# Kernel optimization log

Measured on AMD Instinct MI355X. Metric: run time of the kernel, lower is better.

Reference implementation:

```python
import jax, jax.numpy as jnp
import numpy as np

NUM_HEADS = 8
CHUNK = 64
TOP_K = 5


def setup_inputs() -> dict:
    key = jax.random.key(0)
    ks = jax.random.split(key, 5)
    D = 512
    x = jax.random.normal(ks[0], (1, 2048, D), dtype=jnp.float32)
    s = 0.02
    Wq = jax.random.normal(ks[1], (D, D), dtype=jnp.float32) * s
    Wk = jax.random.normal(ks[2], (D, D), dtype=jnp.float32) * s
    Wv = jax.random.normal(ks[3], (D, D), dtype=jnp.float32) * s
    Wo = jax.random.normal(ks[4], (D, D), dtype=jnp.float32) * s
    return {"x": x, "Wq": Wq, "Wk": Wk, "Wv": Wv, "Wo": Wo}


def reference(x, Wq, Wk, Wv, Wo):
    B, S, D = x.shape
    H = NUM_HEADS
    hd = D // H
    scale = hd ** -0.5
    C = S // CHUNK  # number of chunks

    def split_heads(t):
        return t.reshape(B, S, H, hd).transpose(0, 2, 1, 3)  # [B,H,S,hd]

    Q = split_heads(x @ Wq)
    K = split_heads(x @ Wk)
    V = split_heads(x @ Wv)

    # chunked K/V: [B,H,C,chunk,hd]
    Kc = K.reshape(B, H, C, CHUNK, hd)
    Vc = V.reshape(B, H, C, CHUNK, hd)

    # chunk descriptors: mean-pooled keys per chunk -> [B,H,C,hd]
    chunk_keys = Kc.mean(axis=3)

    # route each query to top-k chunks by scaled similarity
    sims = jnp.einsum('bhsd,bhcd->bhsc', Q, chunk_keys) * scale  # [B,H,S,C]
    _, idx = jax.lax.top_k(sims, TOP_K)  # [B,H,S,K]

    # gather selected K/V chunk blocks: [B,H,S,K,chunk,hd]
    idx_flat = idx.reshape(B, H, S * TOP_K)[:, :, :, None, None]
    Kg = jnp.take_along_axis(Kc, idx_flat, axis=2).reshape(B, H, S, TOP_K, CHUNK, hd)
    Vg = jnp.take_along_axis(Vc, idx_flat, axis=2).reshape(B, H, S, TOP_K, CHUNK, hd)

    # sparse block attention over the K*chunk gathered keys per query
    scores = jnp.einsum('bhsd,bhskcd->bhskc', Q, Kg) * scale
    attn = jax.nn.softmax(scores.reshape(B, H, S, TOP_K * CHUNK), axis=-1)
    attn = attn.reshape(B, H, S, TOP_K, CHUNK)
    out = jnp.einsum('bhskc,bhskcd->bhsd', attn, Vg)  # [B,H,S,hd]

    out = out.transpose(0, 2, 1, 3).reshape(B, S, D)
    return out @ Wo
```

## Files before the change

### kernel.cpp

```cpp
#include <hip/hip_runtime.h>
#include <hip/hip_bf16.h>
#include <math.h>

#define S_LEN 2048
#define D_DIM 512
#define H_NUM 8
#define HD    64
#define C_NUM 32
#define TOPK  5
#define SCALE 0.125f
#define QCAP  1024
#define ATILES 16

typedef __attribute__((ext_vector_type(8))) short bf16x8;
typedef __attribute__((ext_vector_type(4))) float f32x4;
typedef __attribute__((ext_vector_type(4))) unsigned short us4;

__device__ __forceinline__ unsigned short f2b(float f) {
    __hip_bfloat16 h = __float2bfloat16(f);
    unsigned short u;
    __builtin_memcpy(&u, &h, 2);
    return u;
}
__device__ __forceinline__ bf16x8 pack8(float4 a, float4 b) {
    bf16x8 r;
    r[0] = (short)f2b(a.x); r[1] = (short)f2b(a.y);
    r[2] = (short)f2b(a.z); r[3] = (short)f2b(a.w);
    r[4] = (short)f2b(b.x); r[5] = (short)f2b(b.y);
    r[6] = (short)f2b(b.z); r[7] = (short)f2b(b.w);
    return r;
}
__device__ __forceinline__ float b2f(unsigned short u) {
    __hip_bfloat16 h;
    __builtin_memcpy(&h, &u, 2);
    return __bfloat162float(h);
}

#define BM 64
#define BN 64
#define BK 32

__device__ __forceinline__ void gemm_body(const float* __restrict__ A,
                                          const float* __restrict__ B,
                                          float* __restrict__ C,
                                          int M, int N, int K,
                                          int bx, int by) {
    __shared__ float As[BK][BM + 4];
    __shared__ float Bs[BK][BN];

    const int t  = threadIdx.x;
    const int tx = t & 15;
    const int ty = t >> 4;
    const int m0 = by * BM;
    const int n0 = bx * BN;

    float4 acc0 = make_float4(0.f,0.f,0.f,0.f);
    float4 acc1 = make_float4(0.f,0.f,0.f,0.f);
    float4 acc2 = make_float4(0.f,0.f,0.f,0.f);
    float4 acc3 = make_float4(0.f,0.f,0.f,0.f);

    const int ar = t >> 3;
    const int ac = (t & 7) * 4;
    const int br = t >> 4;
    const int bc = (t & 15) * 4;

    float4 a0, a1, b0, b1;
    auto LD = [&](int k0) {
        a0 = *(const float4*)&A[(size_t)(m0 + ar)      * K + k0 + ac];
        a1 = *(const float4*)&A[(size_t)(m0 + ar + 32) * K + k0 + ac];
        b0 = *(const float4*)&B[(size_t)(k0 + br)      * N + n0 + bc];
        b1 = *(const float4*)&B[(size_t)(k0 + br + 16) * N + n0 + bc];
    };

    LD(0);
    for (int k0 = 0; k0 < K; k0 += BK) {
        __syncthreads();
        As[ac+0][ar]    = a0.x; As[ac+1][ar]    = a0.y; As[ac+2][ar]    = a0.z; As[ac+3][ar]    = a0.w;
        As[ac+0][ar+32] = a1.x; As[ac+1][ar+32] = a1.y; As[ac+2][ar+32] = a1.z; As[ac+3][ar+32] = a1.w;
        *(float4*)&Bs[br][bc]      = b0;
        *(float4*)&Bs[br + 16][bc] = b1;
        __syncthreads();

        if (k0 + BK < K) LD(k0 + BK);

        #pragma unroll
        for (int kk = 0; kk < BK; ++kk) {
            float4 a = *(const float4*)&As[kk][ty * 4];
            float4 b = *(const float4*)&Bs[kk][tx * 4];
            acc0.x += a.x*b.x; acc0.y += a.x*b.y; acc0.z += a.x*b.z; acc0.w += a.x*b.w;
            acc1.x += a.y*b.x; acc1.y += a.y*b.y; acc1.z += a.y*b.z; acc1.w += a.y*b.w;
            acc2.x += a.z*b.x; acc2.y += a.z*b.y; acc2.z += a.z*b.z; acc2.w += a.z*b.w;
            acc3.x += a.w*b.x; acc3.y += a.w*b.y; acc3.z += a.w*b.z; acc3.w += a.w*b.w;
        }
    }

    *(float4*)&C[(size_t)(m0 + ty*4 + 0) * N + n0 + tx*4] = acc0;
    *(float4*)&C[(size_t)(m0 + ty*4 + 1) * N + n0 + tx*4] = acc1;
    *(float4*)&C[(size_t)(m0 + ty*4 + 2) * N + n0 + tx*4] = acc2;
    *(float4*)&C[(size_t)(m0 + ty*4 + 3) * N + n0 + tx*4] = acc3;
}

__global__ __launch_bounds__(256) void gemm_qkv(const float* __restrict__ A,
                                                const float* __restrict__ Wq,
                                                const float* __restrict__ Wk,
                                                float* __restrict__ Qb,
                                                float* __restrict__ Kb) {
    const float* B = (blockIdx.z == 0) ? Wq : Wk;
    float*       C = (blockIdx.z == 0) ? Qb : Kb;
    gemm_body(A, B, C, S_LEN, D_DIM, D_DIM, blockIdx.x, blockIdx.y);
}

template <bool ABF16, bool CBF16>
__device__ __forceinline__ void gemm_bf16_body(const void* __restrict__ Aptr,
                                               const float* __restrict__ B,
                                               void* __restrict__ Cptr,
                                               int M, int N, int K,
                                               int bx, int by) {
    __shared__ unsigned short As[64][72];
    __shared__ unsigned short Bs[64][72];

    const int t  = threadIdx.x;
    const int m0 = by * 64;
    const int n0 = bx * 64;
    const int rl = t >> 2;
    const int c4 = (t & 3) * 16;

    const int lane = t & 63, w = t >> 6, lr = lane & 15, quad = lane >> 4;

    f32x4 acc[4] = {{0.f,0.f,0.f,0.f},{0.f,0.f,0.f,0.f},
                    {0.f,0.f,0.f,0.f},{0.f,0.f,0.f,0.f}};

    float4 fa[4]; bf16x8 ba[2]; float4 fb[4];
    auto LDA = [&](int k0) {
        if (ABF16) {
            const unsigned short* A = (const unsigned short*)Aptr;
            ba[0] = *(const bf16x8*)&A[(size_t)(m0 + rl) * K + k0 + c4];
            ba[1] = *(const bf16x8*)&A[(size_t)(m0 + rl) * K + k0 + c4 + 8];
        } else {
            const float* A = (const float*)Aptr;
            const float* p = &A[(size_t)(m0 + rl) * K + k0 + c4];
            fa[0] = *(const float4*)&p[0];  fa[1] = *(const float4*)&p[4];
            fa[2] = *(const float4*)&p[8];  fa[3] = *(const float4*)&p[12];
        }
    };
    auto LDB = [&](int k0) {
        const float* p = &B[(size_t)(k0 + rl) * N + n0 + c4];
        fb[0] = *(const float4*)&p[0];  fb[1] = *(const float4*)&p[4];
        fb[2] = *(const float4*)&p[8];  fb[3] = *(const float4*)&p[12];
    };

    LDA(0); LDB(0);
    for (int k0 = 0; k0 < K; k0 += 64) {
        __syncthreads();
        if (ABF16) {
            *(bf16x8*)&As[rl][c4]     = ba[0];
            *(bf16x8*)&As[rl][c4 + 8] = ba[1];
        } else {
            *(bf16x8*)&As[rl][c4]     = pack8(fa[0], fa[1]);
            *(bf16x8*)&As[rl][c4 + 8] = pack8(fa[2], fa[3]);
        }
        #pragma unroll
        for (int f = 0; f < 4; ++f) {
            float4 v = fb[f];
            Bs[c4 + f*4 + 0][rl] = f2b(v.x);
            Bs[c4 + f*4 + 1][rl] = f2b(v.y);
            Bs[c4 + f*4 + 2][rl] = f2b(v.z);
            Bs[c4 + f*4 + 3][rl] = f2b(v.w);
        }
        __syncthreads();

        if (k0 + 64 < K) { LDA(k0 + 64); LDB(k0 + 64); }

        bf16x8 a0 = *(const bf16x8*)&As[w * 16 + lr][quad * 8];
        bf16x8 a1 = *(const bf16x8*)&As[w * 16 + lr][32 + quad * 8];
        #pragma unroll
        for (int nt = 0; nt < 4; ++nt) {
            bf16x8 b0 = *(const bf16x8*)&Bs[nt * 16 + lr][quad * 8];
            bf16x8 b1 = *(const bf16x8*)&Bs[nt * 16 + lr][32 + quad * 8];
            acc[nt] = __builtin_amdgcn_mfma_f32_16x16x32_bf16(a0, b0, acc[nt], 0, 0, 0);
            acc[nt] = __builtin_amdgcn_mfma_f32_16x16x32_bf16(a1, b1, acc[nt], 0, 0, 0);
        }
    }

    #pragma unroll
    for (int nt = 0; nt < 4; ++nt)
        #pragma unroll
        for (int r = 0; r < 4; ++r) {
            int m = m0 + w * 16 + quad * 4 + r;
            int n = n0 + nt * 16 + lr;
            if (CBF16) ((unsigned short*)Cptr)[(size_t)m * N + n] = f2b(acc[nt][r]);
            else       ((float*)Cptr)[(size_t)m * N + n] = acc[nt][r];
        }
}

__global__ __launch_bounds__(256) void gemm_v(const float* __restrict__ x,
                                              const float* __restrict__ Wv,
                                              unsigned short* __restrict__ Vbf,
                                              int* __restrict__ cur) {
    if (blockIdx.x == 0 && blockIdx.y == 0) cur[threadIdx.x] = 0;
    gemm_bf16_body<false, true>(x, Wv, Vbf, S_LEN, D_DIM, D_DIM,
                                blockIdx.x, blockIdx.y);
}

__global__ __launch_bounds__(256) void gemm_out(const unsigned short* __restrict__ Obn,
                                                const float* __restrict__ Wo,
                                                float* __restrict__ out) {
    gemm_bf16_body<true, false>(Obn, Wo, out, S_LEN, D_DIM, D_DIM,
                                blockIdx.x, blockIdx.y);
}

__global__ __launch_bounds__(256) void chunk_keys_kernel(const float* __restrict__ K,
                                                         float* __restrict__ ck) {
    int i = blockIdx.x * 256 + threadIdx.x;
    int c = i >> 9;
    int d = i & 511;
    const float* p = K + (size_t)c * 64 * D_DIM + d;
    float sum = 0.f;
    #pragma unroll
    for (int r = 0; r < 64; ++r) sum += p[(size_t)r * D_DIM];
    ck[(size_t)c * D_DIM + d] = sum * (1.0f / 64.0f);
}

__global__ __launch_bounds__(256) void sims_topk(const float* __restrict__ Q,
                                                 const float* __restrict__ ck,
                                                 int* __restrict__ cur,
                                                 unsigned short* __restrict__ qlist) {
    __shared__ float qtile[64][68];
    __shared__ float cks[32][68];
    __shared__ float simsb[64][36];
    __shared__ int   lds_cnt[32];
    __shared__ int   lds_base[32];

    const int t  = threadIdx.x;
    const int s0 = blockIdx.x * 64;
    const int h  = blockIdx.y;

    if (t < 32) lds_cnt[t] = 0;

    {
        int r = t >> 2;
        #pragma unroll
        for (int i = 0; i < 4; ++i) {
            int cf4 = (t & 3) * 4 + i;
            *(float4*)&qtile[r][cf4 * 4] =
                *(const float4*)&Q[(size_t)(s0 + r) * D_DIM + h * HD + cf4 * 4];
        }
    }
    for (int i = t; i < C_NUM * 16; i += 256) {
        int c = i >> 4, df4 = i & 15;
        *(float4*)&cks[c][df4 * 4] =
            *(const float4*)&ck[(size_t)c * D_DIM + h * HD + df4 * 4];
    }
    __syncthreads();

    {
        const int sl = t >> 2, g = t & 3;
        float sa[8] = {0.f,0.f,0.f,0.f,0.f,0.f,0.f,0.f};
        #pragma unroll
        for (int d4 = 0; d4 < 16; ++d4) {
            float4 q4 = *(const float4*)&qtile[sl][d4 * 4];
            #pragma unroll
            for (int j = 0; j < 8; ++j) {
                float4 c4 = *(const float4*)&cks[g * 8 + j][d4 * 4];
                sa[j] += q4.x*c4.x + q4.y*c4.y + q4.z*c4.z + q4.w*c4.w;
            }
        }
        *(float4*)&simsb[sl][g*8 + 0] = make_float4(sa[0], sa[1], sa[2], sa[3]);
        *(float4*)&simsb[sl][g*8 + 4] = make_float4(sa[4], sa[5], sa[6], sa[7]);
    }
    __syncthreads();

    int csel[TOPK], lpos[TOPK];
    if (t < 64) {
        float sv[32];
        #pragma unroll
        for (int cq = 0; cq < 8; ++cq) {
            float4 v = *(const float4*)&simsb[t][cq * 4];
            sv[cq*4+0] = v.x; sv[cq*4+1] = v.y; sv[cq*4+2] = v.z; sv[cq*4+3] = v.w;
        }
        #pragma unroll
        for (int k = 0; k < TOPK; ++k) {
            float best = -INFINITY; int bi = 0;
            #pragma unroll
            for (int cc = 0; cc < 32; ++cc) {
                bool gt = sv[cc] > best;
                best = gt ? sv[cc] : best;
                bi   = gt ? cc : bi;
            }
            #pragma unroll
            for (int cc = 0; cc < 32; ++cc)
                if (cc == bi) sv[cc] = -INFINITY;
            csel[k] = bi;
            lpos[k] = atomicAdd(&lds_cnt[bi], 1);
        }
    }
    __syncthreads();

    if (t < 32) lds_base[t] = atomicAdd(&cur[h * 32 + t], lds_cnt[t]);
    __syncthreads();

    if (t < 64) {
        #pragma unroll
        for (int k = 0; k < TOPK; ++k) {
            int c = csel[k];
            int pos = lds_base[c] + lpos[k];
            if (pos < QCAP)
                qlist[(size_t)(h * 32 + c) * QCAP + pos] =
                    (unsigned short)((s0 + t) | (k << 11));
        }
    }
}

__global__ __launch_bounds__(256) void moc_attn6(const float* __restrict__ Q,
                                                 const float* __restrict__ K,
                                                 const unsigned short* __restrict__ Vbf,
                                                 const int* __restrict__ cnt,
                                                 const unsigned short* __restrict__ qlist,
                                                 float* __restrict__ lpart,
                                                 float* __restrict__ Opart) {
    __shared__ unsigned short Qs[64][72];
    __shared__ unsigned short Ks[64][72];
    __shared__ unsigned short VT[64][72];
    __shared__ unsigned short Ps[64][72];
    __shared__ unsigned short slist[64];

    const int hc = blockIdx.y;
    const int h  = hc >> 5;
    const int c  = hc & 31;
    const int g  = blockIdx.x;
    const int t  = threadIdx.x;

    const int count = min(cnt[hc], QCAP);
    const int base  = g * 64;
    if (base >= count) return;
    const int lim = min(count - base, 64);

    const float* Kb = K + ((size_t)c * 64) * D_DIM + h * HD;
    const unsigned short* Vb = Vbf + ((size_t)c * 64) * D_DIM + h * HD;
    const unsigned short* list = qlist + (size_t)hc * QCAP + base;

    {
        const int j  = t >> 2;
        const int d0 = (t & 3) * 16;

        const float* kr = Kb + (size_t)j * D_DIM + d0;
        float4 k0 = *(const float4*)&kr[0],  k1 = *(const float4*)&kr[4];
        float4 k2 = *(const float4*)&kr[8],  k3 = *(const float4*)&kr[12];
        *(bf16x8*)&Ks[j][d0]     = pack8(k0, k1);
        *(bf16x8*)&Ks[j][d0 + 8] = pack8(k2, k3);

        const unsigned short* vr = Vb + (size_t)j * D_DIM + d0;
        bf16x8 v0 = *(const bf16x8*)&vr[0];
        bf16x8 v1 = *(const bf16x8*)&vr[8];
        #pragma unroll
        for (int i = 0; i < 8; ++i) {
            VT[d0 + i][j]     = (unsigned short)v0[i];
            VT[d0 + 8 + i][j] = (unsigned short)v1[i];
        }

        unsigned short pv = (j < lim) ? list[j] : (unsigned short)0xFFFF;
        if ((t & 3) == 0) slist[j] = pv;
        int s = (pv == 0xFFFF) ? 0 : (int)(pv & 2047);
        const float* qr = Q + (size_t)s * D_DIM + h * HD + d0;
        float4 q0 = *(const float4*)&qr[0],  q1 = *(const float4*)&qr[4];
        float4 q2 = *(const float4*)&qr[8],  q3 = *(const float4*)&qr[12];
        *(bf16x8*)&Qs[j][d0]     = pack8(q0, q1);
        *(bf16x8*)&Qs[j][d0 + 8] = pack8(q2, q3);
    }
    __syncthreads();

    const int lane = t & 63;
    const int w    = t >> 6;
    const int lr   = lane & 15;
    const int quad = lane >> 4;

    bf16x8 aq0 = *(const bf16x8*)&Qs[w * 16 + lr][quad * 8];
    bf16x8 aq1 = *(const bf16x8*)&Qs[w * 16 + lr][32 + quad * 8];

    f32x4 acc[4];
    #pragma unroll
    for (int kt = 0; kt < 4; ++kt) {
        bf16x8 b0 = *(const bf16x8*)&Ks[kt * 16 + lr][quad * 8];
        bf16x8 b1 = *(const bf16x8*)&Ks[kt * 16 + lr][32 + quad * 8];
        f32x4 z = {0.f, 0.f, 0.f, 0.f};
        z = __builtin_amdgcn_mfma_f32_16x16x32_bf16(aq0, b0, z, 0, 0, 0);
        z = __builtin_amdgcn_mfma_f32_16x16x32_bf16(aq1, b1, z, 0, 0, 0);
        acc[kt] = z;
    }

    unsigned short pb[4][4];
    float dsum[4] = {0.f, 0.f, 0.f, 0.f};
    #pragma unroll
    for (int kt = 0; kt < 4; ++kt) {
        #pragma unroll
        for (int r = 0; r < 4; ++r) {
            unsigned short u = f2b(__expf(acc[kt][r] * SCALE));
            pb[kt][r] = u;
            dsum[r] += b2f(u);
        }
    }
    #pragma unroll
    for (int r = 0; r < 4; ++r) {
        float v = dsum[r];
        v += __shfl_xor(v, 1, 64);
        v += __shfl_xor(v, 2, 64);
        v += __shfl_xor(v, 4, 64);
        v += __shfl_xor(v, 8, 64);
        dsum[r] = v;
    }
    if (lr == 0) {
        #pragma unroll
        for (int r = 0; r < 4; ++r) {
            unsigned short sv = slist[w * 16 + quad * 4 + r];
            if (sv != 0xFFFF) {
                int kk = sv >> 11, s = sv & 2047;
                lpart[((size_t)kk * H_NUM + h) * S_LEN + s] = dsum[r];
            }
        }
    }

    #pragma unroll
    for (int kt = 0; kt < 4; ++kt)
        #pragma unroll
        for (int r = 0; r < 4; ++r)
            Ps[w * 16 + quad * 4 + r][kt * 16 + lr] = pb[kt][r];

    bf16x8 ap0 = *(const bf16x8*)&Ps[w * 16 + lr][quad * 8];
    bf16x8 ap1 = *(const bf16x8*)&Ps[w * 16 + lr][32 + quad * 8];

    #pragma unroll
    for (int dt = 0; dt < 4; ++dt) {
        bf16x8 b0 = *(const bf16x8*)&VT[dt * 16 + lr][quad * 8];
        bf16x8 b1 = *(const bf16x8*)&VT[dt * 16 + lr][32 + quad * 8];
        f32x4 z = {0.f, 0.f, 0.f, 0.f};
        z = __builtin_amdgcn_mfma_f32_16x16x32_bf16(ap0, b0, z, 0, 0, 0);
        z = __builtin_amdgcn_mfma_f32_16x16x32_bf16(ap1, b1, z, 0, 0, 0);
        #pragma unroll
        for (int r = 0; r < 4; ++r) {
            unsigned short sv = slist[w * 16 + quad * 4 + r];
            if (sv != 0xFFFF) {
                int kk = sv >> 11, s = sv & 2047;
                Opart[((((size_t)kk * H_NUM + h) * S_LEN + s) * HD) + dt * 16 + lr] = z[r];
            }
        }
    }
}

__global__ __launch_bounds__(256) void reduce_norm(const float4* __restrict__ Opart4,
                                                   const float* __restrict__ lpart,
                                                   unsigned short* __restrict__ Obn) {
    int i = blockIdx.x * 256 + threadIdx.x;
    int s    = i >> 7;
    int col4 = i & 127;
    int h    = col4 >> 4;
    int f4   = col4 & 15;
    float4 acc = make_float4(0.f,0.f,0.f,0.f);
    float  den = 0.f;
    #pragma unroll
    for (int k = 0; k < TOPK; ++k) {
        size_t slot = ((size_t)k * H_NUM + h) * S_LEN + s;
        float4 v = Opart4[slot * 16 + f4];
        acc.x += v.x; acc.y += v.y; acc.z += v.z; acc.w += v.w;
        den += lpart[slot];
    }
    float inv = 1.0f / den;
    us4 o;
    o[0] = f2b(acc.x * inv); o[1] = f2b(acc.y * inv);
    o[2] = f2b(acc.z * inv); o[3] = f2b(acc.w * inv);
    *(us4*)&Obn[(size_t)i * 4] = o;
}

extern "C" void kernel_launch(void* const* d_in, const int* in_sizes, int n_in,
                              void* d_out, int out_size, void* d_ws, size_t ws_size,
                              hipStream_t stream) {
    const float* x  = (const float*)d_in[0];
    const float* Wq = (const float*)d_in[1];
    const float* Wk = (const float*)d_in[2];
    const float* Wv = (const float*)d_in[3];
    const float* Wo = (const float*)d_in[4];
    float* out = (float*)d_out;

    const size_t SD = (size_t)S_LEN * D_DIM;
    float* ws    = (float*)d_ws;
    float* Qb    = ws;
    float* Kb    = Qb + SD;
    unsigned short* Vbf = (unsigned short*)(Kb + SD);
    float* ck    = (float*)(Vbf + SD);
    float* lpart = ck + (size_t)C_NUM * D_DIM;
    int*   curb  = (int*)(lpart + (size_t)TOPK * H_NUM * S_LEN);
    unsigned short* qlst = (unsigned short*)(curb + 256);
    float* Opart = (float*)(qlst + (size_t)256 * QCAP);
    unsigned short* Obn = (unsigned short*)Qb;

    dim3 qkgrid(D_DIM / BN, S_LEN / BM, 2);
    gemm_qkv<<<qkgrid, 256, 0, stream>>>(x, Wq, Wk, Qb, Kb);

    dim3 vgrid(D_DIM / 64, S_LEN / 64);
    gemm_v<<<vgrid, 256, 0, stream>>>(x, Wv, Vbf, curb);

    chunk_keys_kernel<<<(C_NUM * D_DIM) / 256, 256, 0, stream>>>(Kb, ck);

    dim3 rgrid(S_LEN / 64, H_NUM);
    sims_topk<<<rgrid, 256, 0, stream>>>(Qb, ck, curb, qlst);

    dim3 agrid(ATILES, H_NUM * C_NUM);
    moc_attn6<<<agrid, 256, 0, stream>>>(Qb, Kb, Vbf, curb, qlst, lpart, Opart);

    reduce_norm<<<(int)(SD / 4 / 256), 256, 0, stream>>>((const float4*)Opart, lpart, Obn);

    dim3 ogrid(D_DIM / 64, S_LEN / 64);
    gemm_out<<<ogrid, 256, 0, stream>>>(Obn, Wo, out);
}
```

Measured before the change: 159.2 us.

## Double-buffer fp32 GEMM shared tiles and merge V projection into QK launch

The fp32 Q/K GEMM now uses two shared-memory buffers, so the next tile is stored while the current one is used, leaving one barrier per k-step instead of two. The separate V projection kernel is merged into the Q/K launch as a third grid slice (blockIdx.z==2), which removes one kernel launch and lets the three projections run at the same time. The cost is double the shared memory in the fp32 path, which may lower occupancy. The merged kernel also declares the shared arrays of both GEMM bodies, which may raise LDS use per block.

```diff
diff --git a/kernel.cpp b/kernel.cpp
--- a/kernel.cpp
+++ b/kernel.cpp
@@ -45,8 +45,8 @@
                                           float* __restrict__ C,
                                           int M, int N, int K,
                                           int bx, int by) {
-    __shared__ float As[BK][BM + 4];
-    __shared__ float Bs[BK][BN];
+    __shared__ float As[2][BK][BM + 4];
+    __shared__ float Bs[2][BK][BN];
 
     const int t  = threadIdx.x;
     const int tx = t & 15;
@@ -71,43 +71,39 @@
         b0 = *(const float4*)&B[(size_t)(k0 + br)      * N + n0 + bc];
         b1 = *(const float4*)&B[(size_t)(k0 + br + 16) * N + n0 + bc];
     };
-
-    LD(0);
+    auto ST = [&](int p) {
+        As[p][ac+0][ar]    = a0.x; As[p][ac+1][ar]    = a0.y; As[p][ac+2][ar]    = a0.z; As[p][ac+3][ar]    = a0.w;
+        As[p][ac+0][ar+32] = a1.x; As[p][ac+1][ar+32] = a1.y; As[p][ac+2][ar+32] = a1.z; As[p][ac+3][ar+32] = a1.w;
+        *(float4*)&Bs[p][br][bc]      = b0;
+        *(float4*)&Bs[p][br + 16][bc] = b1;
+    };
+
+    LD(0); ST(0); __syncthreads();
+
+    int p = 0;
     for (int k0 = 0; k0 < K; k0 += BK) {
-        __syncthreads();
-        As[ac+0][ar]    = a0.x; As[ac+1][ar]    = a0.y; As[ac+2][ar]    = a0.z; As[ac+3][ar]    = a0.w;
-        As[ac+0][ar+32] = a1.x; As[ac+1][ar+32] = a1.y; As[ac+2][ar+32] = a1.z; As[ac+3][ar+32] = a1.w;
-        *(float4*)&Bs[br][bc]      = b0;
-        *(float4*)&Bs[br + 16][bc] = b1;
-        __syncthreads();
-
-        if (k0 + BK < K) LD(k0 + BK);
+        const bool more = (k0 + BK < K);
+        if (more) LD(k0 + BK);
 
         #pragma unroll
         for (int kk = 0; kk < BK; ++kk) {
-            float4 a = *(const float4*)&As[kk][ty * 4];
-            float4 b = *(const float4*)&Bs[kk][tx * 4];
+            float4 a = *(const float4*)&As[p][kk][ty * 4];
+            float4 b = *(const float4*)&Bs[p][kk][tx * 4];
             acc0.x += a.x*b.x; acc0.y += a.x*b.y; acc0.z += a.x*b.z; acc0.w += a.x*b.w;
             acc1.x += a.y*b.x; acc1.y += a.y*b.y; acc1.z += a.y*b.z; acc1.w += a.y*b.w;
             acc2.x += a.z*b.x; acc2.y += a.z*b.y; acc2.z += a.z*b.z; acc2.w += a.z*b.w;
             acc3.x += a.w*b.x; acc3.y += a.w*b.y; acc3.z += a.w*b.z; acc3.w += a.w*b.w;
         }
+
+        if (more) ST(p ^ 1);
+        __syncthreads();
+        p ^= 1;
     }
 
     *(float4*)&C[(size_t)(m0 + ty*4 + 0) * N + n0 + tx*4] = acc0;
     *(float4*)&C[(size_t)(m0 + ty*4 + 1) * N + n0 + tx*4] = acc1;
     *(float4*)&C[(size_t)(m0 + ty*4 + 2) * N + n0 + tx*4] = acc2;
     *(float4*)&C[(size_t)(m0 + ty*4 + 3) * N + n0 + tx*4] = acc3;
-}
-
-__global__ __launch_bounds__(256) void gemm_qkv(const float* __restrict__ A,
-                                                const float* __restrict__ Wq,
-                                                const float* __restrict__ Wk,
-                                                float* __restrict__ Qb,
-                                                float* __restrict__ Kb) {
-    const float* B = (blockIdx.z == 0) ? Wq : Wk;
-    float*       C = (blockIdx.z == 0) ? Qb : Kb;
-    gemm_body(A, B, C, S_LEN, D_DIM, D_DIM, blockIdx.x, blockIdx.y);
 }
 
 template <bool ABF16, bool CBF16>
@@ -193,13 +189,23 @@
         }
 }
 
-__global__ __launch_bounds__(256) void gemm_v(const float* __restrict__ x,
-                                              const float* __restrict__ Wv,
-                                              unsigned short* __restrict__ Vbf,
-                                              int* __restrict__ cur) {
-    if (blockIdx.x == 0 && blockIdx.y == 0) cur[threadIdx.x] = 0;
-    gemm_bf16_body<false, true>(x, Wv, Vbf, S_LEN, D_DIM, D_DIM,
-                                blockIdx.x, blockIdx.y);
+__global__ __launch_bounds__(256) void gemm_qkv(const float* __restrict__ x,
+                                                const float* __restrict__ Wq,
+                                                const float* __restrict__ Wk,
+                                                const float* __restrict__ Wv,
+                                                float* __restrict__ Qb,
+                                                float* __restrict__ Kb,
+                                                unsigned short* __restrict__ Vbf,
+                                                int* __restrict__ cur) {
+    if (blockIdx.z == 2) {
+        if (blockIdx.x == 0 && blockIdx.y == 0) cur[threadIdx.x] = 0;
+        gemm_bf16_body<false, true>(x, Wv, Vbf, S_LEN, D_DIM, D_DIM,
+                                    blockIdx.x, blockIdx.y);
+        return;
+    }
+    const float* B = (blockIdx.z == 0) ? Wq : Wk;
+    float*       C = (blockIdx.z == 0) ? Qb : Kb;
+    gemm_body(x, B, C, S_LEN, D_DIM, D_DIM, blockIdx.x, blockIdx.y);
 }
 
 __global__ __launch_bounds__(256) void gemm_out(const unsigned short* __restrict__ Obn,
@@ -492,11 +498,8 @@
     float* Opart = (float*)(qlst + (size_t)256 * QCAP);
     unsigned short* Obn = (unsigned short*)Qb;
 
-    dim3 qkgrid(D_DIM / BN, S_LEN / BM, 2);
-    gemm_qkv<<<qkgrid, 256, 0, stream>>>(x, Wq, Wk, Qb, Kb);
-
-    dim3 vgrid(D_DIM / 64, S_LEN / 64);
-    gemm_v<<<vgrid, 256, 0, stream>>>(x, Wv, Vbf, curb);
+    dim3 qkvgrid(D_DIM / BN, S_LEN / BM, 3);
+    gemm_qkv<<<qkvgrid, 256, 0, stream>>>(x, Wq, Wk, Wv, Qb, Kb, Vbf, curb);
 
     chunk_keys_kernel<<<(C_NUM * D_DIM) / 256, 256, 0, stream>>>(Kb, ck);
 
```

After: 169.1 us. 1.06x slower.

## Double-buffer A tile in LDS and stream B directly from global in registers

Applied to the files above, without the earlier changes.

The fp32 GEMM body now keeps the A tile in a double-buffered LDS array and drops the B shared-memory tile. Each thread instead loads its B column slice straight from global memory into two ping-pong register arrays of 8 float4, prefetching the next 8 rows while computing on the current ones. This removes one barrier per K step and the B LDS traffic, and overlaps global loads with FMA work. In exchange it adds register pressure and redundant global B loads across threads that share columns, which rely on L1/L2 hits.

```diff
diff --git a/kernel.cpp b/kernel.cpp
--- a/kernel.cpp
+++ b/kernel.cpp
@@ -40,13 +40,18 @@
 #define BN 64
 #define BK 32
 
+#define FMA16(a, b)                                                          \
+    acc0.x += a.x*b.x; acc0.y += a.x*b.y; acc0.z += a.x*b.z; acc0.w += a.x*b.w; \
+    acc1.x += a.y*b.x; acc1.y += a.y*b.y; acc1.z += a.y*b.z; acc1.w += a.y*b.w; \
+    acc2.x += a.z*b.x; acc2.y += a.z*b.y; acc2.z += a.z*b.z; acc2.w += a.z*b.w; \
+    acc3.x += a.w*b.x; acc3.y += a.w*b.y; acc3.z += a.w*b.z; acc3.w += a.w*b.w;
+
 __device__ __forceinline__ void gemm_body(const float* __restrict__ A,
                                           const float* __restrict__ B,
                                           float* __restrict__ C,
                                           int M, int N, int K,
                                           int bx, int by) {
-    __shared__ float As[BK][BM + 4];
-    __shared__ float Bs[BK][BN];
+    __shared__ float As[2][BK][BM + 4];
 
     const int t  = threadIdx.x;
     const int tx = t & 15;
@@ -61,38 +66,64 @@
 
     const int ar = t >> 3;
     const int ac = (t & 7) * 4;
-    const int br = t >> 4;
-    const int bc = (t & 15) * 4;
-
-    float4 a0, a1, b0, b1;
-    auto LD = [&](int k0) {
+
+    float4 a0, a1;
+    auto LDA = [&](int k0) {
         a0 = *(const float4*)&A[(size_t)(m0 + ar)      * K + k0 + ac];
         a1 = *(const float4*)&A[(size_t)(m0 + ar + 32) * K + k0 + ac];
-        b0 = *(const float4*)&B[(size_t)(k0 + br)      * N + n0 + bc];
-        b1 = *(const float4*)&B[(size_t)(k0 + br + 16) * N + n0 + bc];
     };
-
-    LD(0);
+    auto STA = [&](int p) {
+        As[p][ac+0][ar]    = a0.x; As[p][ac+1][ar]    = a0.y; As[p][ac+2][ar]    = a0.z; As[p][ac+3][ar]    = a0.w;
+        As[p][ac+0][ar+32] = a1.x; As[p][ac+1][ar+32] = a1.y; As[p][ac+2][ar+32] = a1.z; As[p][ac+3][ar+32] = a1.w;
+    };
+
+    const float* Bcol = B + n0 + tx * 4;
+    float4 b0[8], b1[8];
+#define LDB8(dst, kb)                                                        \
+    {                                                                        \
+        _Pragma("unroll")                                                    \
+        for (int j = 0; j < 8; ++j)                                          \
+            dst[j] = *(const float4*)&Bcol[(size_t)((kb) + j) * N];          \
+    }
+
+    LDA(0); STA(0);
+    LDB8(b0, 0);
+    __syncthreads();
+
+    int p = 0;
     for (int k0 = 0; k0 < K; k0 += BK) {
+        const bool more = (k0 + BK < K);
+        if (more) LDA(k0 + BK);
+
+        #pragma unroll
+        for (int g = 0; g < 4; ++g) {
+            const int kn = k0 + g * 8 + 8;
+            if ((g & 1) == 0) {
+                if (kn < K) LDB8(b1, kn);
+                #pragma unroll
+                for (int j = 0; j < 8; ++j) {
+                    const int kk = g * 8 + j;
+                    float4 a = *(const float4*)&As[p][kk][ty * 4];
+                    float4 b = b0[j];
+                    FMA16(a, b)
+                }
+            } else {
+                if (kn < K) LDB8(b0, kn);
+                #pragma unroll
+                for (int j = 0; j < 8; ++j) {
+                    const int kk = g * 8 + j;
+                    float4 a = *(const float4*)&As[p][kk][ty * 4];
+                    float4 b = b1[j];
+                    FMA16(a, b)
+                }
+            }
+        }
+
+        if (more) STA(p ^ 1);
         __syncthreads();
-        As[ac+0][ar]    = a0.x; As[ac+1][ar]    = a0.y; As[ac+2][ar]    = a0.z; As[ac+3][ar]    = a0.w;
-        As[ac+0][ar+32] = a1.x; As[ac+1][ar+32] = a1.y; As[ac+2][ar+32] = a1.z; As[ac+3][ar+32] = a1.w;
-        *(float4*)&Bs[br][bc]      = b0;
-        *(float4*)&Bs[br + 16][bc] = b1;
-        __syncthreads();
-
-        if (k0 + BK < K) LD(k0 + BK);
-
-        #pragma unroll
-        for (int kk = 0; kk < BK; ++kk) {
-            float4 a = *(const float4*)&As[kk][ty * 4];
-            float4 b = *(const float4*)&Bs[kk][tx * 4];
-            acc0.x += a.x*b.x; acc0.y += a.x*b.y; acc0.z += a.x*b.z; acc0.w += a.x*b.w;
-            acc1.x += a.y*b.x; acc1.y += a.y*b.y; acc1.z += a.y*b.z; acc1.w += a.y*b.w;
-            acc2.x += a.z*b.x; acc2.y += a.z*b.y; acc2.z += a.z*b.z; acc2.w += a.z*b.w;
-            acc3.x += a.w*b.x; acc3.y += a.w*b.y; acc3.z += a.w*b.z; acc3.w += a.w*b.w;
-        }
-    }
+        p ^= 1;
+    }
+#undef LDB8
 
     *(float4*)&C[(size_t)(m0 + ty*4 + 0) * N + n0 + tx*4] = acc0;
     *(float4*)&C[(size_t)(m0 + ty*4 + 1) * N + n0 + tx*4] = acc1;
```

Result: slower. 185.5 us (+16.5%).
